# Kernel optimization log

Measured on AMD Instinct MI355X. Metric: run time of the kernel, lower is better.

## Reference

```python
import jax, jax.numpy as jnp
import numpy as np
from jax import lax

BN_EPS = 1e-5


def setup_inputs() -> dict:
    key = jax.random.key(0)
    ks = jax.random.split(key, 4)
    T, N, I, H, O, K = 2048, 16, 1024, 2048, 1024, 12
    return {
        "inputs": jax.random.normal(ks[0], (T, N, I), dtype=jnp.float32),
        "wv": jax.random.normal(ks[1], (H, I), dtype=jnp.float32) * (1.0 / np.sqrt(I)),
        "gamma": jnp.ones((H,), dtype=jnp.float32),
        "beta": jnp.zeros((H,), dtype=jnp.float32),
        "wu": jax.random.normal(ks[2], (O, H), dtype=jnp.float32) * (1.0 / np.sqrt(H)),
        "bu": jnp.zeros((O,), dtype=jnp.float32),
        "memory_weights": jax.random.normal(ks[3], (K, H), dtype=jnp.float32) * 0.05,
        "stride": 2,
        "l_memory_size": 10,
        "r_memory_size": 1,
    }


def _memory_block(p, memory_weights, stride, l_mem, r_mem):
    # p: [N, T, H]. p_hatt[n,t,h] = sum_k w[k,h] * p[n, t + (k-l_mem)*stride, h]
    # == depthwise 1D cross-correlation with dilation=stride, 'same' asymmetric pad.
    H = p.shape[-1]
    x = jnp.transpose(p, (0, 2, 1))              # [N, H, T]
    kern = memory_weights.T[:, None, :]          # [H, 1, K]
    out = lax.conv_general_dilated(
        x, kern,
        window_strides=(1,),
        padding=[(l_mem * stride, r_mem * stride)],
        rhs_dilation=(stride,),
        dimension_numbers=("NCH", "OIH", "NCH"),
        feature_group_count=H,
    )
    return jnp.transpose(out, (0, 2, 1))         # [N, T, H]


def reference(inputs, wv, gamma, beta, wu, bu, memory_weights,
              stride, l_memory_size, r_memory_size):
    # wx_v then transpose(0,1): [T,N,I] -> [N,T,H]
    p = jnp.einsum("tni,hi->nth", inputs, wv)
    p_hatt = p + _memory_block(p, memory_weights, stride, l_memory_size, r_memory_size)
    # SequenceWise(BatchNorm1d) in train mode: stats over flattened (N*T) rows.
    H = p_hatt.shape[-1]
    flat = p_hatt.reshape(-1, H)
    mean = flat.mean(axis=0)
    var = flat.var(axis=0)  # biased, matches torch BN normalization
    xn = (p_hatt - mean) * lax.rsqrt(var + BN_EPS) * gamma + beta
    h = jax.nn.relu(jnp.einsum("nth,oh->nto", xn, wu) + bu)
    return (h, p_hatt)
```

## Files before the change

kernel.cpp:

```cpp
#include <hip/hip_runtime.h>
#include <hip/hip_bf16.h>
#include <stdint.h>

#define T_DIM 2048
#define N_DIM 16
#define I_DIM 1024
#define H_DIM 2048
#define O_DIM 1024
#define K_TAPS 12
#define MROWS (N_DIM * T_DIM)
#define BN_EPS 1e-5f

#define S_LEN 1024
#define TCHUNK 48
#define SCHUNKS 22

typedef __attribute__((ext_vector_type(8))) short bf16x8;
typedef __attribute__((ext_vector_type(4))) float f32x4;

__device__ __forceinline__ unsigned short f2bf_rne(float f) {
    union { float f; unsigned u; } v; v.f = f;
    unsigned u = v.u;
    unsigned r = u + 0x7fffu + ((u >> 16) & 1u);
    return (unsigned short)(r >> 16);
}

__device__ __forceinline__ float bf2f(unsigned short x) {
    union { unsigned u; float f; } v; v.u = ((unsigned)x) << 16; return v.f;
}

__device__ __forceinline__ bf16x8 pack8(const float4& a, const float4& b) {
    bf16x8 v;
    v[0] = (short)f2bf_rne(a.x); v[1] = (short)f2bf_rne(a.y);
    v[2] = (short)f2bf_rne(a.z); v[3] = (short)f2bf_rne(a.w);
    v[4] = (short)f2bf_rne(b.x); v[5] = (short)f2bf_rne(b.y);
    v[6] = (short)f2bf_rne(b.z); v[7] = (short)f2bf_rne(b.w);
    return v;
}

__global__ void cvt_kernel(const float* __restrict__ in, unsigned short* __restrict__ out, int n4) {
    int i = blockIdx.x * blockDim.x + threadIdx.x;
    int stride = gridDim.x * blockDim.x;
    for (; i < n4; i += stride) {
        float4 v = ((const float4*)in)[i];
        ushort4 o;
        o.x = f2bf_rne(v.x); o.y = f2bf_rne(v.y);
        o.z = f2bf_rne(v.z); o.w = f2bf_rne(v.w);
        ((ushort4*)out)[i] = o;
    }
}

__device__ __forceinline__ void gload_lds16(const void* g, void* l) {
    __builtin_amdgcn_global_load_lds(
        (const __attribute__((address_space(1))) unsigned int*)g,
        (__attribute__((address_space(3))) unsigned int*)l, 16, 0, 0);
}

template<int PERM, int EPI, int KD, int NCOLS>
__global__ __launch_bounds__(512, 2) void gemm256(
    const float* __restrict__ A,
    const unsigned short* __restrict__ B,
    void* __restrict__ Cout,
    const float* __restrict__ bias)
{
    __shared__ char lds[131072];

    const int tid  = threadIdx.x;
    const int wid  = tid >> 6;
    const int lane = tid & 63;
    const int wr   = (wid >> 2) * 128;
    const int wc   = (wid & 3) * 64;
    const int fr   = lane & 15;
    const int fh   = lane >> 4;

    const int nwg = gridDim.x;
    const int lin = blockIdx.x;
    const int tile = (lin & 7) * (nwg >> 3) + (lin >> 3);
    const int ntx = NCOLS / 256;
    const long c0 = (long)(tile % ntx) * 256;
    const long r0 = (long)(tile / ntx) * 256;

    long aBase, aStride;
    if (PERM) {
        const long n0 = r0 / T_DIM;
        const long t0 = r0 % T_DIM;
        aBase = (t0 * N_DIM + n0) * (long)KD;
        aStride = (long)N_DIM * KD;
    } else {
        aBase = r0 * (long)KD;
        aStride = KD;
    }
    const long bBase = c0 * (long)KD;

    auto stageB = [&](int buf, int si, int kt) {
        const int row = si * 64 + (tid >> 3);
        const int g   = (tid & 7) ^ (row & 7);
        const long gelem = bBase + (long)row * (long)KD + (long)kt * 64 + g * 8;
        gload_lds16((const char*)B + gelem * 2,
                    lds + buf * 65536 + 32768 + si * 8192 + tid * 16);
    };

    auto loadA = [&](float4* dst, int wi, int kt) {
        const int row = wi * 64 + (tid >> 3);
        const long base = aBase + (long)row * aStride + (long)kt * 64 + (tid & 7) * 8;
        dst[0] = *(const float4*)(A + base);
        dst[1] = *(const float4*)(A + base + 4);
    };
    auto writeA = [&](int buf, int wi, const float4* src) {
        const int row = wi * 64 + (tid >> 3);
        const int blk = tid & 7;
        *(bf16x8*)(lds + buf * 65536 + row * 128 + (((blk ^ (row & 7))) << 4)) =
            pack8(src[0], src[1]);
    };

    auto rdA = [&](int buf, int m, int ks) -> bf16x8 {
        const int row = wr + m * 16 + fr;
        const int blk = ks * 4 + fh;
        return *(const bf16x8*)(lds + buf * 65536 + row * 128 + ((blk ^ (row & 7)) << 4));
    };
    auto rdB = [&](int buf, int n, int ks) -> bf16x8 {
        const int row = wc + n * 16 + fr;
        const int blk = ks * 4 + fh;
        return *(const bf16x8*)(lds + buf * 65536 + 32768 + row * 128 + ((blk ^ (row & 7)) << 4));
    };

    f32x4 acc[8][4] = {};
    float4 aA[8], aB[8];

    stageB(0, 0, 0); stageB(0, 1, 0); stageB(0, 2, 0); stageB(0, 3, 0);
    loadA(&aA[0], 0, 0); loadA(&aA[2], 1, 0); loadA(&aA[4], 2, 0); loadA(&aA[6], 3, 0);
    writeA(0, 0, &aA[0]); writeA(0, 1, &aA[2]); writeA(0, 2, &aA[4]); writeA(0, 3, &aA[6]);
    loadA(&aB[0], 0, 1); loadA(&aB[2], 1, 1); loadA(&aB[4], 2, 1); loadA(&aB[6], 3, 1);
    asm volatile("s_waitcnt vmcnt(8) lgkmcnt(0)" ::: "memory");
    __builtin_amdgcn_s_barrier();

    const int KT  = KD / 64;
    const int KT2 = KT / 2;
    for (int i = 0; i < KT2; ++i) {
        const bool haveNext = (i + 1 < KT2);
        const int tB1 = 2 * i + 1, tN = 2 * i + 2, tNN = 2 * i + 3;

        {
            bf16x8 bfr[4][2];
#pragma unroll
            for (int q = 0; q < 4; ++q) {
                writeA(1, q, &aB[2 * q]);
                if (q == 0) { stageB(1, 0, tB1); stageB(1, 1, tB1); stageB(1, 2, tB1); stageB(1, 3, tB1); }
                if (haveNext) loadA(&aA[2 * q], q, tN);
                if (q == 0) {
#pragma unroll
                    for (int n = 0; n < 4; ++n)
#pragma unroll
                        for (int ks = 0; ks < 2; ++ks) bfr[n][ks] = rdB(0, n, ks);
                }
                bf16x8 af[2][2];
#pragma unroll
                for (int mm = 0; mm < 2; ++mm)
#pragma unroll
                    for (int ks = 0; ks < 2; ++ks) af[mm][ks] = rdA(0, q * 2 + mm, ks);
                __builtin_amdgcn_s_setprio(1);
#pragma unroll
                for (int mm = 0; mm < 2; ++mm)
#pragma unroll
                    for (int n = 0; n < 4; ++n)
#pragma unroll
                        for (int ks = 0; ks < 2; ++ks)
                            acc[q * 2 + mm][n] = __builtin_amdgcn_mfma_f32_16x16x32_bf16(
                                af[mm][ks], bfr[n][ks], acc[q * 2 + mm][n], 0, 0, 0);
                __builtin_amdgcn_s_setprio(0);
                if (q == 3) {
                    if (haveNext) asm volatile("s_waitcnt vmcnt(8) lgkmcnt(0)" ::: "memory");
                    else          asm volatile("s_waitcnt vmcnt(0) lgkmcnt(0)" ::: "memory");
                }
                __builtin_amdgcn_s_barrier();
            }
        }

        {
            bf16x8 bfr[4][2];
#pragma unroll
            for (int q = 0; q < 4; ++q) {
                if (haveNext) {
                    writeA(0, q, &aA[2 * q]);
                    if (q == 0) { stageB(0, 0, tN); stageB(0, 1, tN); stageB(0, 2, tN); stageB(0, 3, tN); }
                    loadA(&aB[2 * q], q, tNN);
                }
                if (q == 0) {
#pragma unroll
                    for (int n = 0; n < 4; ++n)
#pragma unroll
                        for (int ks = 0; ks < 2; ++ks) bfr[n][ks] = rdB(1, n, ks);
                }
                bf16x8 af[2][2];
#pragma unroll
                for (int mm = 0; mm < 2; ++mm)
#pragma unroll
                    for (int ks = 0; ks < 2; ++ks) af[mm][ks] = rdA(1, q * 2 + mm, ks);
                __builtin_amdgcn_s_setprio(1);
#pragma unroll
                for (int mm = 0; mm < 2; ++mm)
#pragma unroll
                    for (int n = 0; n < 4; ++n)
#pragma unroll
                        for (int ks = 0; ks < 2; ++ks)
                            acc[q * 2 + mm][n] = __builtin_amdgcn_mfma_f32_16x16x32_bf16(
                                af[mm][ks], bfr[n][ks], acc[q * 2 + mm][n], 0, 0, 0);
                __builtin_amdgcn_s_setprio(0);
                if (q == 3) {
                    if (haveNext) asm volatile("s_waitcnt vmcnt(8) lgkmcnt(0)" ::: "memory");
                    else          asm volatile("s_waitcnt vmcnt(0) lgkmcnt(0)" ::: "memory");
                }
                __builtin_amdgcn_s_barrier();
            }
        }
    }

#pragma unroll
    for (int m = 0; m < 8; ++m) {
        const long orow_base = r0 + wr + m * 16 + fh * 4;
#pragma unroll
        for (int n = 0; n < 4; ++n) {
            const long ocol = c0 + wc + n * 16 + fr;
#pragma unroll
            for (int j = 0; j < 4; ++j) {
                const long orow = orow_base + j;
                float vv = acc[m][n][j];
                if (EPI == 0) {
                    ((unsigned short*)Cout)[orow * NCOLS + ocol] = f2bf_rne(vv);
                } else {
                    vv += bias[ocol];
                    vv = vv > 0.f ? vv : 0.f;
                    ((float*)Cout)[orow * NCOLS + ocol] = vv;
                }
            }
        }
    }
}

__global__ __launch_bounds__(256) void conv_bn_v3(
    const unsigned short* __restrict__ p,
    const float* __restrict__ w,
    float* __restrict__ ph_f32,
    float* __restrict__ sums)
{
    const int tid   = threadIdx.x;
    const int b     = blockIdx.x;
    const int half  = b & 1;
    const int chunk = (b >> 1) % SCHUNKS;
    const int np    = (b >> 1) / SCHUNKS;
    const int par   = np & 1;
    const int n     = np >> 1;
    const int h0    = half * 1024 + tid * 4;

    float wk[12][4];
#pragma unroll
    for (int k = 0; k < 12; ++k) {
        float4 v = *(const float4*)&w[k * H_DIM + h0];
        wk[k][0] = v.x; wk[k][1] = v.y; wk[k][2] = v.z; wk[k][3] = v.w;
    }

    const long b0 = ((long)n * T_DIM + par) * (long)H_DIM + h0;
    const int s0 = chunk * TCHUNK;

    float win[12][4];
#pragma unroll
    for (int j = 0; j < 12; ++j) {
        const int s = s0 + j - 10;
        if (s >= 0 && s < S_LEN) {
            ushort4 v = *(const ushort4*)&p[b0 + (long)s * (2 * H_DIM)];
            win[j][0] = bf2f(v.x); win[j][1] = bf2f(v.y);
            win[j][2] = bf2f(v.z); win[j][3] = bf2f(v.w);
        } else {
            win[j][0] = 0.f; win[j][1] = 0.f; win[j][2] = 0.f; win[j][3] = 0.f;
        }
    }

    float st1[4] = {0.f, 0.f, 0.f, 0.f};
    float st2[4] = {0.f, 0.f, 0.f, 0.f};

    for (int ss = 0; ss < TCHUNK; ss += 12) {
#pragma unroll
        for (int uu = 0; uu < 12; ++uu) {
            const int s = s0 + ss + uu;
            if (s < S_LEN) {
                float out[4];
#pragma unroll
                for (int c = 0; c < 4; ++c) out[c] = win[(uu + 10) % 12][c];
#pragma unroll
                for (int k = 0; k < 12; ++k)
#pragma unroll
                    for (int c = 0; c < 4; ++c)
                        out[c] += wk[k][c] * win[(uu + k) % 12][c];

                const long base = b0 + (long)s * (2 * H_DIM);
                *(float4*)&ph_f32[base] = make_float4(out[0], out[1], out[2], out[3]);
#pragma unroll
                for (int c = 0; c < 4; ++c) { st1[c] += out[c]; st2[c] += out[c] * out[c]; }
            }
            {
                const int sn = s0 + ss + uu + 2;
                if (sn < S_LEN) {
                    ushort4 v = *(const ushort4*)&p[b0 + (long)sn * (2 * H_DIM)];
                    win[uu][0] = bf2f(v.x); win[uu][1] = bf2f(v.y);
                    win[uu][2] = bf2f(v.z); win[uu][3] = bf2f(v.w);
                } else {
                    win[uu][0] = 0.f; win[uu][1] = 0.f; win[uu][2] = 0.f; win[uu][3] = 0.f;
                }
            }
        }
    }

#pragma unroll
    for (int c = 0; c < 4; ++c) {
        atomicAdd(&sums[h0 + c], st1[c]);
        atomicAdd(&sums[H_DIM + h0 + c], st2[c]);
    }
}

__global__ void bn_finalize(const float* __restrict__ sums,
                            const float* __restrict__ gamma,
                            const float* __restrict__ beta,
                            float* __restrict__ sshift) {
    int h = blockIdx.x * blockDim.x + threadIdx.x;
    if (h >= H_DIM) return;
    float mean = sums[h] * (1.f / (float)MROWS);
    float var  = sums[H_DIM + h] * (1.f / (float)MROWS) - mean * mean;
    float s = gamma[h] * rsqrtf(var + BN_EPS);
    sshift[h] = s;
    sshift[H_DIM + h] = beta[h] - mean * s;
}

__global__ void scale_wu(const float* __restrict__ wu,
                         const float* __restrict__ sshift,
                         unsigned short* __restrict__ wu2) {
    int idx = blockIdx.x * blockDim.x + threadIdx.x;
    int stride = gridDim.x * blockDim.x;
    for (; idx < O_DIM * H_DIM; idx += stride) {
        int h = idx & (H_DIM - 1);
        wu2[idx] = f2bf_rne(wu[idx] * sshift[h]);
    }
}

__global__ __launch_bounds__(256) void bias2_kernel(
    const float* __restrict__ wu,
    const float* __restrict__ sshift,
    const float* __restrict__ bu,
    float* __restrict__ bias2) {
    const int o = blockIdx.x;
    float part = 0.f;
    for (int h = threadIdx.x; h < H_DIM; h += 256)
        part += sshift[H_DIM + h] * wu[(long)o * H_DIM + h];
#pragma unroll
    for (int off = 32; off > 0; off >>= 1) part += __shfl_down(part, off, 64);
    __shared__ float red[4];
    const int wv = threadIdx.x >> 6, lane = threadIdx.x & 63;
    if (lane == 0) red[wv] = part;
    __syncthreads();
    if (threadIdx.x == 0) bias2[o] = bu[o] + red[0] + red[1] + red[2] + red[3];
}

extern "C" void kernel_launch(void* const* d_in, const int* in_sizes, int n_in,
                              void* d_out, int out_size, void* d_ws, size_t ws_size,
                              hipStream_t stream) {
    const float* inputs = (const float*)d_in[0];
    const float* wv     = (const float*)d_in[1];
    const float* gamma  = (const float*)d_in[2];
    const float* beta   = (const float*)d_in[3];
    const float* wu     = (const float*)d_in[4];
    const float* bu     = (const float*)d_in[5];
    const float* mw     = (const float*)d_in[6];

    float* out_h  = (float*)d_out;
    float* out_ph = out_h + (size_t)MROWS * O_DIM;

    unsigned short* p_b = (unsigned short*)d_out;

    char* ws = (char*)d_ws;
    unsigned short* wv_b  = (unsigned short*)(ws + 201326592);
    unsigned short* wu2_b = (unsigned short*)(ws + 205520896);
    float* sums   = (float*)(ws + 209715200);
    float* sshift = (float*)(ws + 209731584);
    float* bias2  = (float*)(ws + 209747968);

    hipMemsetAsync(sums, 0, 2 * H_DIM * sizeof(float), stream);

    cvt_kernel<<<512, 256, 0, stream>>>(wv, wv_b, (H_DIM * I_DIM) / 4);

    gemm256<1, 0, I_DIM, H_DIM><<<(MROWS / 256) * (H_DIM / 256), 512, 0, stream>>>(
        inputs, wv_b, (void*)p_b, nullptr);

    conv_bn_v3<<<2 * SCHUNKS * 2 * N_DIM, 256, 0, stream>>>(p_b, mw, out_ph, sums);

    bn_finalize<<<(H_DIM + 255) / 256, 256, 0, stream>>>(sums, gamma, beta, sshift);
    scale_wu<<<2048, 256, 0, stream>>>(wu, sshift, wu2_b);
    bias2_kernel<<<O_DIM, 256, 0, stream>>>(wu, sshift, bu, bias2);

    gemm256<0, 1, H_DIM, O_DIM><<<(MROWS / 256) * (O_DIM / 256), 512, 0, stream>>>(
        out_ph, wu2_b, (void*)out_h, bias2);
}
```

Baseline: 498.0 us.

## Emit bf16 copy of p_hatt in conv and use all-bf16 DMA GEMM for output

The conv/BN kernel now also writes a bf16 copy of p_hatt to workspace. The second GEMM is a new variant that reads this bf16 A with direct global-to-LDS loads instead of loading fp32 into registers and converting. It also uses a restructured half-tile staging pipeline with setprio around MFMA. This roughly halves the second GEMM's A-operand traffic and removes the conversion work, at the cost of an extra 128 MB write in the conv kernel.

```diff
diff --git a/kernel.cpp b/kernel.cpp
--- a/kernel.cpp
+++ b/kernel.cpp
@@ -57,7 +57,7 @@
 }
 
 template<int PERM, int EPI, int KD, int NCOLS>
-__global__ __launch_bounds__(512, 2) void gemm256(
+__global__ __launch_bounds__(512, 2) void gemm256_a32(
     const float* __restrict__ A,
     const unsigned short* __restrict__ B,
     void* __restrict__ Cout,
@@ -99,7 +99,6 @@
         gload_lds16((const char*)B + gelem * 2,
                     lds + buf * 65536 + 32768 + si * 8192 + tid * 16);
     };
-
     auto loadA = [&](float4* dst, int wi, int kt) {
         const int row = wi * 64 + (tid >> 3);
         const long base = aBase + (long)row * aStride + (long)kt * 64 + (tid & 7) * 8;
@@ -112,7 +111,6 @@
         *(bf16x8*)(lds + buf * 65536 + row * 128 + (((blk ^ (row & 7))) << 4)) =
             pack8(src[0], src[1]);
     };
-
     auto rdA = [&](int buf, int m, int ks) -> bf16x8 {
         const int row = wr + m * 16 + fr;
         const int blk = ks * 4 + fh;
@@ -237,10 +235,178 @@
     }
 }
 
-__global__ __launch_bounds__(256) void conv_bn_v3(
+template<int PERM, int EPI, int KD, int NCOLS>
+__global__ __launch_bounds__(512, 2) void gemm256(
+    const unsigned short* __restrict__ A,
+    const unsigned short* __restrict__ B,
+    void* __restrict__ Cout,
+    const float* __restrict__ bias)
+{
+    __shared__ char lds[131072];
+
+    const int tid  = threadIdx.x;
+    const int wid  = tid >> 6;
+    const int lane = tid & 63;
+    const int wr   = (wid >> 2) * 128;
+    const int wc   = (wid & 3) * 64;
+    const int fr   = lane & 15;
+    const int fh   = lane >> 4;
+
+    const int nwg = gridDim.x;
+    const int lin = blockIdx.x;
+    const int tile = (lin & 7) * (nwg >> 3) + (lin >> 3);
+    const int ntx = NCOLS / 256;
+    const long c0 = (long)(tile % ntx) * 256;
+    const long r0 = (long)(tile / ntx) * 256;
+
+    long aBase, aStride;
+    if (PERM) {
+        const long n0 = r0 / T_DIM;
+        const long t0 = r0 % T_DIM;
+        aBase = (t0 * N_DIM + n0) * (long)KD;
+        aStride = (long)N_DIM * KD;
+    } else {
+        aBase = r0 * (long)KD;
+        aStride = KD;
+    }
+    const long bBase = c0 * (long)KD;
+
+    auto stage_half = [&](int buf, int mat, int h, int kt) {
+        char* mbase = lds + buf * 65536 + mat * 32768 + h * 16384;
+#pragma unroll
+        for (int j = 0; j < 2; ++j) {
+            const int row = h * 128 + j * 64 + (tid >> 3);
+            const int g   = (tid & 7) ^ (row & 7);
+            long gelem;
+            if (mat == 0) gelem = aBase + (long)row * aStride + (long)kt * 64 + g * 8;
+            else          gelem = bBase + (long)row * (long)KD + (long)kt * 64 + g * 8;
+            gload_lds16((const char*)(mat == 0 ? A : B) + gelem * 2,
+                        mbase + j * 8192 + tid * 16);
+        }
+    };
+
+    auto rdA = [&](int buf, int m, int ks) -> bf16x8 {
+        const int row = wr + m * 16 + fr;
+        const int blk = ks * 4 + fh;
+        return *(const bf16x8*)(lds + buf * 65536 + row * 128 + ((blk ^ (row & 7)) << 4));
+    };
+    auto rdB = [&](int buf, int n, int ks) -> bf16x8 {
+        const int row = wc + n * 16 + fr;
+        const int blk = ks * 4 + fh;
+        return *(const bf16x8*)(lds + buf * 65536 + 32768 + row * 128 + ((blk ^ (row & 7)) << 4));
+    };
+
+    f32x4 acc[8][4] = {};
+
+    stage_half(0, 0, 0, 0); stage_half(0, 0, 1, 0);
+    stage_half(0, 1, 0, 0); stage_half(0, 1, 1, 0);
+
+    const int KT  = KD / 64;
+    const int KT2 = KT / 2;
+    for (int i = 0; i < KT2; ++i) {
+        const int tB = 2 * i + 1;
+        const bool haveNext = (i + 1 < KT2);
+        bf16x8 bfr[4][2];
+
+#pragma unroll
+        for (int q = 0; q < 4; ++q) {
+            stage_half(1, q >> 1, q & 1, tB);
+            bf16x8 af[2][2];
+            if (q == 0) {
+                asm volatile("s_waitcnt vmcnt(2)" ::: "memory");
+                __builtin_amdgcn_s_barrier();
+#pragma unroll
+                for (int n = 0; n < 4; ++n)
+#pragma unroll
+                    for (int ks = 0; ks < 2; ++ks) bfr[n][ks] = rdB(0, n, ks);
+#pragma unroll
+                for (int mm = 0; mm < 2; ++mm)
+#pragma unroll
+                    for (int ks = 0; ks < 2; ++ks) af[mm][ks] = rdA(0, q * 2 + mm, ks);
+            } else {
+#pragma unroll
+                for (int mm = 0; mm < 2; ++mm)
+#pragma unroll
+                    for (int ks = 0; ks < 2; ++ks) af[mm][ks] = rdA(0, q * 2 + mm, ks);
+                __builtin_amdgcn_s_barrier();
+            }
+            __builtin_amdgcn_s_setprio(1);
+#pragma unroll
+            for (int mm = 0; mm < 2; ++mm)
+#pragma unroll
+                for (int n = 0; n < 4; ++n)
+#pragma unroll
+                    for (int ks = 0; ks < 2; ++ks)
+                        acc[q * 2 + mm][n] = __builtin_amdgcn_mfma_f32_16x16x32_bf16(
+                            af[mm][ks], bfr[n][ks], acc[q * 2 + mm][n], 0, 0, 0);
+            __builtin_amdgcn_s_setprio(0);
+            __builtin_amdgcn_s_barrier();
+        }
+
+#pragma unroll
+        for (int q = 0; q < 4; ++q) {
+            if (haveNext) stage_half(0, q >> 1, q & 1, 2 * i + 2);
+            bf16x8 af[2][2];
+            if (q == 0) {
+                if (haveNext) asm volatile("s_waitcnt vmcnt(2)" ::: "memory");
+                else          asm volatile("s_waitcnt vmcnt(0)" ::: "memory");
+                __builtin_amdgcn_s_barrier();
+#pragma unroll
+                for (int n = 0; n < 4; ++n)
+#pragma unroll
+                    for (int ks = 0; ks < 2; ++ks) bfr[n][ks] = rdB(1, n, ks);
+#pragma unroll
+                for (int mm = 0; mm < 2; ++mm)
+#pragma unroll
+                    for (int ks = 0; ks < 2; ++ks) af[mm][ks] = rdA(1, q * 2 + mm, ks);
+            } else {
+#pragma unroll
+                for (int mm = 0; mm < 2; ++mm)
+#pragma unroll
+                    for (int ks = 0; ks < 2; ++ks) af[mm][ks] = rdA(1, q * 2 + mm, ks);
+                __builtin_amdgcn_s_barrier();
+            }
+            __builtin_amdgcn_s_setprio(1);
+#pragma unroll
+            for (int mm = 0; mm < 2; ++mm)
+#pragma unroll
+                for (int n = 0; n < 4; ++n)
+#pragma unroll
+                    for (int ks = 0; ks < 2; ++ks)
+                        acc[q * 2 + mm][n] = __builtin_amdgcn_mfma_f32_16x16x32_bf16(
+                            af[mm][ks], bfr[n][ks], acc[q * 2 + mm][n], 0, 0, 0);
+            __builtin_amdgcn_s_setprio(0);
+            __builtin_amdgcn_s_barrier();
+        }
+    }
+
+#pragma unroll
+    for (int m = 0; m < 8; ++m) {
+        const long orow_base = r0 + wr + m * 16 + fh * 4;
+#pragma unroll
+        for (int n = 0; n < 4; ++n) {
+            const long ocol = c0 + wc + n * 16 + fr;
+#pragma unroll
+            for (int j = 0; j < 4; ++j) {
+                const long orow = orow_base + j;
+                float vv = acc[m][n][j];
+                if (EPI == 0) {
+                    ((unsigned short*)Cout)[orow * NCOLS + ocol] = f2bf_rne(vv);
+                } else {
+                    vv += bias[ocol];
+                    vv = vv > 0.f ? vv : 0.f;
+                    ((float*)Cout)[orow * NCOLS + ocol] = vv;
+                }
+            }
+        }
+    }
+}
+
+__global__ __launch_bounds__(256) void conv_bn_v2(
     const unsigned short* __restrict__ p,
     const float* __restrict__ w,
     float* __restrict__ ph_f32,
+    unsigned short* __restrict__ ph_b,
     float* __restrict__ sums)
 {
     const int tid   = threadIdx.x;
@@ -294,6 +460,10 @@
 
                 const long base = b0 + (long)s * (2 * H_DIM);
                 *(float4*)&ph_f32[base] = make_float4(out[0], out[1], out[2], out[3]);
+                ushort4 ob;
+                ob.x = f2bf_rne(out[0]); ob.y = f2bf_rne(out[1]);
+                ob.z = f2bf_rne(out[2]); ob.w = f2bf_rne(out[3]);
+                *(ushort4*)&ph_b[base] = ob;
 #pragma unroll
                 for (int c = 0; c < 4; ++c) { st1[c] += out[c]; st2[c] += out[c] * out[c]; }
             }
@@ -376,6 +546,7 @@
     unsigned short* p_b = (unsigned short*)d_out;
 
     char* ws = (char*)d_ws;
+    unsigned short* ph_b  = (unsigned short*)ws;
     unsigned short* wv_b  = (unsigned short*)(ws + 201326592);
     unsigned short* wu2_b = (unsigned short*)(ws + 205520896);
     float* sums   = (float*)(ws + 209715200);
@@ -386,15 +557,15 @@
 
     cvt_kernel<<<512, 256, 0, stream>>>(wv, wv_b, (H_DIM * I_DIM) / 4);
 
-    gemm256<1, 0, I_DIM, H_DIM><<<(MROWS / 256) * (H_DIM / 256), 512, 0, stream>>>(
+    gemm256_a32<1, 0, I_DIM, H_DIM><<<(MROWS / 256) * (H_DIM / 256), 512, 0, stream>>>(
         inputs, wv_b, (void*)p_b, nullptr);
 
-    conv_bn_v3<<<2 * SCHUNKS * 2 * N_DIM, 256, 0, stream>>>(p_b, mw, out_ph, sums);
+    conv_bn_v2<<<2 * SCHUNKS * 2 * N_DIM, 256, 0, stream>>>(p_b, mw, out_ph, ph_b, sums);
 
     bn_finalize<<<(H_DIM + 255) / 256, 256, 0, stream>>>(sums, gamma, beta, sshift);
     scale_wu<<<2048, 256, 0, stream>>>(wu, sshift, wu2_b);
     bias2_kernel<<<O_DIM, 256, 0, stream>>>(wu, sshift, bu, bias2);
 
     gemm256<0, 1, H_DIM, O_DIM><<<(MROWS / 256) * (O_DIM / 256), 512, 0, stream>>>(
-        out_ph, wu2_b, (void*)out_h, bias2);
-}
+        ph_b, wu2_b, (void*)out_h, bias2);
+}
```

Measured after the change: 474.5 us. 4.7% less time.
